# Performance work log

Measured on AMD Instinct MI355X. Metric: run time of the kernel, lower is better.

## Reference

```python
import jax, jax.numpy as jnp
import numpy as np

B, N, IN_DIM, HID, OUT, E = 2, 50000, 64, 256, 128, 500000

def setup_inputs() -> dict:
    key = jax.random.key(0)
    ks = jax.random.split(key, 8)
    s = lambda fan_in: 1.0 / np.sqrt(fan_in)
    x = jax.random.normal(ks[0], (B, N, IN_DIM), dtype=jnp.float32)
    edges = jax.random.randint(ks[1], (E, 2), 0, N, dtype=jnp.int64)
    return {
        "x": x,
        "edges": edges,
        "ew1": jax.random.normal(ks[2], (2 * IN_DIM, HID), dtype=jnp.float32) * s(2 * IN_DIM),
        "eb1": jnp.zeros((HID,), jnp.float32),
        "ew2": jax.random.normal(ks[3], (HID, OUT), dtype=jnp.float32) * s(HID),
        "eb2": jnp.zeros((OUT,), jnp.float32),
        "nw1": jax.random.normal(ks[4], (IN_DIM, HID), dtype=jnp.float32) * s(IN_DIM),
        "nb1": jnp.zeros((HID,), jnp.float32),
        "nw2": jax.random.normal(ks[5], (HID, OUT), dtype=jnp.float32) * s(HID),
        "nb2": jnp.zeros((OUT,), jnp.float32),
        "dw": jax.random.normal(ks[6], (OUT, IN_DIM), dtype=jnp.float32) * s(OUT),
        "db": jnp.zeros((IN_DIM,), jnp.float32),
    }

def _mlp(z, w1, b1, w2, b2):
    return jax.nn.relu(z @ w1 + b1) @ w2 + b2

def reference(x, edges, ew1, eb1, ew2, eb2, nw1, nb1, nw2, nb2, dw, db):
    u, v = edges[:, 0], edges[:, 1]
    # node embedding: [B, N, OUT]
    h = _mlp(x, nw1, nb1, nw2, nb2)
    # per-edge MLP on concatenated endpoint features: [B, E, OUT]
    edge_input = jnp.concatenate([x[:, u], x[:, v]], axis=-1)  # [B, E, 2*IN]
    edge_emb = _mlp(edge_input, ew1, eb1, ew2, eb2)
    # scatter-add edge message to both endpoints
    messages = jnp.zeros_like(h).at[:, u].add(edge_emb).at[:, v].add(edge_emb)
    h = h + messages
    recon = h @ dw + db  # [B, N, IN]
    return recon
```

## Files before the change

### kernel.cpp

```cpp
#include <hip/hip_runtime.h>
#include <hip/hip_bf16.h>

#define BB   2
#define NN   50000
#define BN   100000
#define NE   500000
#define NSB  196

using u16 = unsigned short;
using u32 = unsigned int;
typedef __attribute__((ext_vector_type(8))) short short8;
typedef __attribute__((ext_vector_type(8))) _Float16 half8;
typedef __attribute__((ext_vector_type(4))) float f32x4;

__device__ __forceinline__ u16 f2bf(float f) {
    union { float f; u32 u; } w; w.f = f;
    return (u16)((w.u + 0x7fffu + ((w.u >> 16) & 1u)) >> 16);
}
__device__ __forceinline__ u16 f2h(float f) {
    _Float16 h = (_Float16)f; u16 u; __builtin_memcpy(&u, &h, 2); return u;
}

#if defined(__has_builtin)
#if __has_builtin(__builtin_amdgcn_cvt_pk_bf16_f32)
#define HAVE_CVTPK 1
#endif
#if __has_builtin(__builtin_amdgcn_cvt_pkrtz)
#define HAVE_PKRTZ 1
#endif
#endif

__device__ __forceinline__ u32 pack_bf(float lo, float hi) {
#ifdef HAVE_CVTPK
    auto r = __builtin_amdgcn_cvt_pk_bf16_f32(lo, hi);
    u32 out; __builtin_memcpy(&out, &r, sizeof(out));
    return out;
#else
    return ((u32)f2bf(hi) << 16) | (u32)f2bf(lo);
#endif
}

__device__ __forceinline__ u32 pack_h2(float lo, float hi) {
#ifdef HAVE_PKRTZ
    auto r = __builtin_amdgcn_cvt_pkrtz(lo, hi);
    u32 out; __builtin_memcpy(&out, &r, sizeof(out));
    return out;
#else
    return ((u32)f2h(hi) << 16) | (u32)f2h(lo);
#endif
}

__device__ __forceinline__ u32 pk_add_h2(u32 a, u32 b) {
    u32 d; asm("v_pk_add_f16 %0, %1, %2" : "=v"(d) : "v"(a), "v"(b)); return d;
}
__device__ __forceinline__ u32 pk_relu_h2(u32 a) {
    u32 d, z = 0u;
    asm("v_pk_max_f16 %0, %1, %2" : "=v"(d) : "v"(a), "v"(z)); return d;
}
__device__ __forceinline__ half8 as_h8(short8 s) {
    half8 h; __builtin_memcpy(&h, &s, 16); return h;
}

__global__ __launch_bounds__(256) void csr_zero2(int* __restrict__ a, int* __restrict__ b) {
    int i = blockIdx.x * 256 + threadIdx.x;
    if (i < NN) { a[i] = 0; b[i] = 0; }
}

__global__ __launch_bounds__(256) void csr_hist2(const int* __restrict__ edges,
                                                 int* __restrict__ curU,
                                                 int* __restrict__ curV) {
    int e = blockIdx.x * 256 + threadIdx.x;
    if (e < NE) {
        atomicAdd(&curU[edges[2*e]], 1);
        atomicAdd(&curV[edges[2*e+1]], 1);
    }
}

__global__ __launch_bounds__(256) void scan_pass1(const int* __restrict__ cursor,
                                                  int* __restrict__ bsum) {
    __shared__ int s[256];
    const int t = threadIdx.x;
    int i = blockIdx.x * 256 + t;
    s[t] = (i < NN) ? cursor[i] : 0;
    __syncthreads();
    for (int d = 128; d > 0; d >>= 1) {
        if (t < d) s[t] += s[t + d];
        __syncthreads();
    }
    if (t == 0) bsum[blockIdx.x] = s[0];
}

__global__ __launch_bounds__(256) void scan_pass2(const int* __restrict__ bsum,
                                                  int* __restrict__ boff) {
    __shared__ int s[256];
    const int t = threadIdx.x;
    s[t] = (t < NSB) ? bsum[t] : 0;
    __syncthreads();
    for (int d = 1; d < 256; d <<= 1) {
        int v = (t >= d) ? s[t - d] : 0;
        __syncthreads();
        s[t] += v;
        __syncthreads();
    }
    if (t <= NSB) boff[t] = (t == 0) ? 0 : s[t - 1];
}

__global__ __launch_bounds__(256) void scan_pass3(int* __restrict__ cursor,
                                                  const int* __restrict__ boff,
                                                  int* __restrict__ off) {
    __shared__ int s[256];
    const int t = threadIdx.x;
    int i = blockIdx.x * 256 + t;
    int v = (i < NN) ? cursor[i] : 0;
    s[t] = v;
    __syncthreads();
    for (int d = 1; d < 256; d <<= 1) {
        int p = (t >= d) ? s[t - d] : 0;
        __syncthreads();
        s[t] += p;
        __syncthreads();
    }
    int excl = boff[blockIdx.x] + s[t] - v;
    if (i < NN) { off[i] = excl; cursor[i] = excl; }
    if (i == NN - 1) off[NN] = excl + v;
}

__global__ __launch_bounds__(256) void csr_fillU(const int* __restrict__ edges,
                                                 int* __restrict__ curU,
                                                 int* __restrict__ ueidx,
                                                 int* __restrict__ upos) {
    int e = blockIdx.x * 256 + threadIdx.x;
    if (e < NE) {
        int s = atomicAdd(&curU[edges[2*e]], 1);
        ueidx[s] = e;
        upos[e] = s;
    }
}

__global__ __launch_bounds__(256) void csr_fillV(const int* __restrict__ edges,
                                                 int* __restrict__ curV,
                                                 const int* __restrict__ upos,
                                                 int* __restrict__ vmap) {
    int e = blockIdx.x * 256 + threadIdx.x;
    if (e < NE) {
        int s = atomicAdd(&curV[edges[2*e+1]], 1);
        vmap[s] = upos[e];
    }
}

__global__ __launch_bounds__(256) void weight_prep(
    const float* __restrict__ ew1, const float* __restrict__ nw1,
    const float* __restrict__ ew2, const float* __restrict__ nw2,
    const float* __restrict__ dw,  const float* __restrict__ db,
    const float* __restrict__ eb2, const float* __restrict__ nb2,
    u16* __restrict__ frag, float* __restrict__ bias2)
{
    int blk = blockIdx.x, t = threadIdx.x;
    if (blk < 192) {
        int idx = blk * 256 + t;
        const float* src; int KB, local;
        if (idx < 32768) { local = idx;         src = ew1; KB = 4; }
        else             { local = idx - 32768; src = nw1; KB = 2; }
        int j = local & 7, l = (local >> 3) & 63, rest = local >> 9;
        int kblk = rest % KB, ntile = rest / KB;
        int n = ntile * 16 + (l & 15);
        int k = kblk * 32 + ((l >> 4) << 3) + j;
        frag[idx] = f2bf(src[k * 256 + n]);
    } else if (blk < 320) {
        int idx = (blk - 192) * 256 + t;
        bool is_e = (idx < 16384);
        const float* src = is_e ? ew2 : nw2;
        int local = idx & 16383;
        int j = local & 7, l = (local >> 3) & 63, rest = local >> 9;
        int kblk = rest & 7, ntile = rest >> 3;
        int n = ntile * 16 + (l & 15);
        int k = kblk * 32 + ((l >> 4) << 3) + j;
        float s = 0.f;
        for (int jj = 0; jj < 128; ++jj) s = fmaf(src[k * 128 + jj], dw[jj * 64 + n], s);
        frag[49152 + idx] = is_e ? f2h(s) : f2bf(s);
    } else if (t < 128) {
        int d = t & 63;
        const float* bsrc = (t >= 64) ? nb2 : eb2;
        float s = 0.f;
        #pragma unroll 4
        for (int j = 0; j < 128; ++j) s = fmaf(bsrc[j], dw[j * 64 + d], s);
        if (t >= 64) bias2[64 + d] = s + db[d];
        else         bias2[d] = s;
    }
}

__global__ __launch_bounds__(256) void node_mlp_kernel(
    const float* __restrict__ x, const float* __restrict__ nb1,
    const float* __restrict__ bias2, const u16* __restrict__ frag,
    u16* __restrict__ xbf, float* __restrict__ out)
{
    __shared__ u16 xs[64 * 64];
    __shared__ u16 hid[64 * 256];
    const int t = threadIdx.x;
    const int wave = t >> 6, l = t & 63, lane15 = l & 15, quad = l >> 4;
    const int r0 = blockIdx.x * 64;
    const int valid = min(64, BN - r0);

    #pragma unroll
    for (int it = 0; it < 4; ++it) {
        int i = t + it * 256;
        int m = i >> 4, c4 = i & 15;
        int row = min(r0 + m, BN - 1);
        float4 g = ((const float4*)x)[(size_t)row * 16 + c4];
        uint2 q = make_uint2(pack_bf(g.x, g.y), pack_bf(g.z, g.w));
        int chunk = c4 >> 1;
        *(uint2*)(xs + m * 64 + ((chunk ^ (m & 7)) << 3) + (c4 & 1) * 4) = q;
        *(uint2*)(xbf + (size_t)row * 64 + c4 * 4) = q;
    }
    __syncthreads();

    {
        f32x4 acc[4][4];
        #pragma unroll
        for (int i = 0; i < 4; ++i)
            #pragma unroll
            for (int mt = 0; mt < 4; ++mt) acc[i][mt] = f32x4{0.f,0.f,0.f,0.f};
        const u16* w1 = frag + 32768;
        #pragma unroll
        for (int kblk = 0; kblk < 2; ++kblk) {
            short8 bf[4], af[4];
            int chunk = kblk * 4 + quad;
            #pragma unroll
            for (int mt = 0; mt < 4; ++mt) {
                int row = mt*16 + lane15;
                bf[mt] = *(const short8*)(xs + row * 64 + ((chunk ^ (row & 7)) << 3));
            }
            #pragma unroll
            for (int i = 0; i < 4; ++i)
                af[i] = *(const short8*)(w1 + (((wave*4 + i)*2 + kblk)*64 + l) * 8);
            #pragma unroll
            for (int i = 0; i < 4; ++i)
                #pragma unroll
                for (int mt = 0; mt < 4; ++mt)
                    acc[i][mt] = __builtin_amdgcn_mfma_f32_16x16x32_bf16(af[i], bf[mt], acc[i][mt], 0, 0, 0);
        }
        #pragma unroll
        for (int i = 0; i < 4; ++i) {
            int n0 = (wave*4 + i)*16 + quad*4;
            int chunk = (wave*4 + i)*2 + (quad >> 1);
            float4 bv = *(const float4*)(nb1 + n0);
            #pragma unroll
            for (int mt = 0; mt < 4; ++mt) {
                int row = mt*16 + lane15;
                uint2 q = make_uint2(
                    pack_bf(fmaxf(acc[i][mt][0] + bv.x, 0.f), fmaxf(acc[i][mt][1] + bv.y, 0.f)),
                    pack_bf(fmaxf(acc[i][mt][2] + bv.z, 0.f), fmaxf(acc[i][mt][3] + bv.w, 0.f)));
                *(uint2*)(hid + row * 256 + ((chunk ^ (row & 15)) << 3) + (quad & 1) * 4) = q;
            }
        }
    }
    __syncthreads();

    {
        f32x4 acc[4];
        #pragma unroll
        for (int mt = 0; mt < 4; ++mt) acc[mt] = f32x4{0.f,0.f,0.f,0.f};
        const u16* w2 = frag + 65536;
        #pragma unroll
        for (int kblk = 0; kblk < 8; ++kblk) {
            short8 bf[4], af;
            int chunk = kblk * 4 + quad;
            #pragma unroll
            for (int mt = 0; mt < 4; ++mt) {
                int row = mt*16 + lane15;
                bf[mt] = *(const short8*)(hid + row * 256 + ((chunk ^ (row & 15)) << 3));
            }
            af = *(const short8*)(w2 + ((wave*8 + kblk)*64 + l) * 8);
            #pragma unroll
            for (int mt = 0; mt < 4; ++mt)
                acc[mt] = __builtin_amdgcn_mfma_f32_16x16x32_bf16(af, bf[mt], acc[mt], 0, 0, 0);
        }
        int n0 = wave*16 + quad*4;
        float4 bv = *(const float4*)(bias2 + 64 + n0);
        #pragma unroll
        for (int mt = 0; mt < 4; ++mt) {
            int m = mt*16 + lane15;
            if (m < valid) {
                float4 o;
                o.x = acc[mt][0] + bv.x; o.y = acc[mt][1] + bv.y;
                o.z = acc[mt][2] + bv.z; o.w = acc[mt][3] + bv.w;
                *(float4*)(out + (size_t)(r0 + m) * 64 + n0) = o;
            }
        }
    }
}

__global__ __launch_bounds__(256) void edge_pre_kernel(
    const u16* __restrict__ xbf, const float* __restrict__ eb1,
    const u16* __restrict__ frag, u16* __restrict__ At, u16* __restrict__ Ab,
    int b)
{
    __shared__ u16 xs[64 * 64];
    __shared__ u16 stg[64 * 256];
    const int t = threadIdx.x;
    const int wave = t >> 6, l = t & 63, lane15 = l & 15, quad = l >> 4;
    const int r0 = blockIdx.x * 64;
    const int valid = min(64, NN - r0);

    #pragma unroll
    for (int it = 0; it < 2; ++it) {
        int i = t + it * 256;
        int m = i >> 3, c = i & 7;
        int row = min(r0 + m, NN - 1);
        uint4 q = ((const uint4*)xbf)[((size_t)(b * NN + row)) * 8 + c];
        *(uint4*)(xs + m * 64 + ((c ^ (m & 7)) << 3)) = q;
    }
    __syncthreads();

    const u16* w1 = frag;
    for (int T = 0; T < 2; ++T) {
        f32x4 acc[4][4];
        #pragma unroll
        for (int i = 0; i < 4; ++i)
            #pragma unroll
            for (int mt = 0; mt < 4; ++mt) acc[i][mt] = f32x4{0.f,0.f,0.f,0.f};
        #pragma unroll
        for (int kblk = 0; kblk < 2; ++kblk) {
            short8 bf[4], af[4];
            int chunk = kblk * 4 + quad;
            #pragma unroll
            for (int mt = 0; mt < 4; ++mt) {
                int row = mt*16 + lane15;
                bf[mt] = *(const short8*)(xs + row * 64 + ((chunk ^ (row & 7)) << 3));
            }
            #pragma unroll
            for (int i = 0; i < 4; ++i)
                af[i] = *(const short8*)(w1 + (((wave*4 + i)*4 + T*2 + kblk)*64 + l) * 8);
            #pragma unroll
            for (int i = 0; i < 4; ++i)
                #pragma unroll
                for (int mt = 0; mt < 4; ++mt)
                    acc[i][mt] = __builtin_amdgcn_mfma_f32_16x16x32_bf16(af[i], bf[mt], acc[i][mt], 0, 0, 0);
        }
        #pragma unroll
        for (int i = 0; i < 4; ++i) {
            int ntile = wave*4 + i;
            int n0 = ntile*16 + quad*4;
            float4 bv;
            if (T == 0) bv = *(const float4*)(eb1 + n0);
            else        bv = make_float4(0.f, 0.f, 0.f, 0.f);
            int c16 = ntile*2 + (quad >> 1);
            #pragma unroll
            for (int mt = 0; mt < 4; ++mt) {
                int row = mt*16 + lane15;
                uint2 q = make_uint2(
                    pack_h2(acc[i][mt][0] + bv.x, acc[i][mt][1] + bv.y),
                    pack_h2(acc[i][mt][2] + bv.z, acc[i][mt][3] + bv.w));
                *(uint2*)(stg + row * 256 + ((c16 ^ (row & 7)) << 3) + (quad & 1) * 4) = q;
            }
        }
        __syncthreads();
        u16* dst = (T == 0) ? At : Ab;
        #pragma unroll
        for (int it = 0; it < 8; ++it) {
            int i = t + it * 256;
            int m = i >> 5, c = i & 31;
            if (m < valid)
                ((uint4*)dst)[((size_t)(r0 + m)) * 32 + c] =
                    *(const uint4*)(stg + m * 256 + ((c ^ (m & 7)) << 3));
        }
        __syncthreads();
    }
}

__global__ __launch_bounds__(256) void edge_emb2_kernel(
    const u16* __restrict__ At, const u16* __restrict__ Ab,
    const int* __restrict__ edges, const int* __restrict__ ueidx,
    const float* __restrict__ bias2,
    const u16* __restrict__ frag, u16* __restrict__ perm)
{
    __shared__ u16 hid[64 * 128];
    __shared__ int us[64], vs[64];
    const int t = threadIdx.x;
    const int wave = t >> 6, l = t & 63, lane15 = l & 15, quad = l >> 4;
    const int e0 = blockIdx.x * 64;
    const int valid = min(64, NE - e0);

    if (t < 64) {
        int j = min(e0 + t, NE - 1);
        int e = ueidx[j];
        us[t] = edges[2 * e];
        vs[t] = edges[2 * e + 1];
    }
    __syncthreads();

    f32x4 acc[4];
    #pragma unroll
    for (int mt = 0; mt < 4; ++mt) acc[mt] = f32x4{0.f,0.f,0.f,0.f};
    const u16* w2 = frag + 49152;

    #pragma unroll
    for (int half = 0; half < 2; ++half) {
        #pragma unroll
        for (int it = 0; it < 4; ++it) {
            int i = t + it * 256;
            int m = i >> 4, c = i & 15;
            int cg = half * 16 + c;
            int u = us[m], v = vs[m];
            uint4 a = ((const uint4*)At)[(size_t)((u32)u) * 32 + cg];
            uint4 bq = ((const uint4*)Ab)[(size_t)((u32)v) * 32 + cg];
            uint4 r;
            r.x = pk_relu_h2(pk_add_h2(a.x, bq.x));
            r.y = pk_relu_h2(pk_add_h2(a.y, bq.y));
            r.z = pk_relu_h2(pk_add_h2(a.z, bq.z));
            r.w = pk_relu_h2(pk_add_h2(a.w, bq.w));
            *(uint4*)(hid + m * 128 + ((c ^ (m & 15)) << 3)) = r;
        }
        __syncthreads();

        #pragma unroll
        for (int kb = 0; kb < 4; ++kb) {
            short8 bf[4], af;
            int chunk = kb * 4 + quad;
            #pragma unroll
            for (int mt = 0; mt < 4; ++mt) {
                int row = mt*16 + lane15;
                bf[mt] = *(const short8*)(hid + row * 128 + ((chunk ^ (row & 15)) << 3));
            }
            af = *(const short8*)(w2 + ((wave*8 + half*4 + kb)*64 + l) * 8);
            #pragma unroll
            for (int mt = 0; mt < 4; ++mt)
                acc[mt] = __builtin_amdgcn_mfma_f32_16x16x32_f16(as_h8(af), as_h8(bf[mt]), acc[mt], 0, 0, 0);
        }
        __syncthreads();
    }

    {
        int n0 = wave*16 + quad*4;
        int chunk = wave*2 + (quad >> 1);
        float4 bv = *(const float4*)(bias2 + n0);
        #pragma unroll
        for (int mt = 0; mt < 4; ++mt) {
            int m = mt*16 + lane15;
            uint2 q = make_uint2(
                pack_bf(acc[mt][0] + bv.x, acc[mt][1] + bv.y),
                pack_bf(acc[mt][2] + bv.z, acc[mt][3] + bv.w));
            *(uint2*)(hid + m * 64 + ((chunk ^ (m & 7)) << 3) + (quad & 1) * 4) = q;
        }
    }
    __syncthreads();

    #pragma unroll
    for (int it = 0; it < 2; ++it) {
        int i = t + it * 256;
        int m = i >> 3, c8 = i & 7;
        if (m < valid)
            ((uint4*)perm)[((size_t)(e0 + m)) * 8 + c8] =
                *(const uint4*)(hid + m * 64 + ((c8 ^ (m & 7)) << 3));
    }
}

__global__ __launch_bounds__(256) void gather3_kernel(
    const u32* __restrict__ perm32, const int* __restrict__ uoff,
    const int* __restrict__ voff, const int* __restrict__ vmap,
    float* __restrict__ out, int b)
{
    const int t = threadIdx.x, wave = t >> 6, l = t & 63;
    const int n = blockIdx.x * 4 + wave;
    const int ub = uoff[n], ucnt = uoff[n + 1] - ub;
    const int vb = voff[n], vcnt = voff[n + 1] - vb;
    if ((ucnt | vcnt) == 0) return;
    const int slot = l >> 4, c8h = l & 15;
    float a0 = 0.f, a1 = 0.f, a2 = 0.f, a3 = 0.f;

    for (int j0 = 0; j0 < ucnt; j0 += 8) {
        int jA = j0 + slot, jB = j0 + 4 + slot;
        const u32* rpA = perm32 + (size_t)(ub + min(jA, ucnt - 1)) * 32 + 2 * c8h;
        const u32* rpB = perm32 + (size_t)(ub + min(jB, ucnt - 1)) * 32 + 2 * c8h;
        u32 wA0 = rpA[0], wA1 = rpA[1];
        u32 wB0 = rpB[0], wB1 = rpB[1];
        union { u32 u; float f; } x0, x1, x2, x3;
        if (jA < ucnt) {
            x0.u = wA0 << 16; x1.u = wA0 & 0xffff0000u;
            x2.u = wA1 << 16; x3.u = wA1 & 0xffff0000u;
            a0 += x0.f; a1 += x1.f; a2 += x2.f; a3 += x3.f;
        }
        if (jB < ucnt) {
            x0.u = wB0 << 16; x1.u = wB0 & 0xffff0000u;
            x2.u = wB1 << 16; x3.u = wB1 & 0xffff0000u;
            a0 += x0.f; a1 += x1.f; a2 += x2.f; a3 += x3.f;
        }
    }
    for (int j0 = 0; j0 < vcnt; j0 += 8) {
        int jA = j0 + slot, jB = j0 + 4 + slot;
        int pA = vmap[vb + min(jA, vcnt - 1)];
        int pB = vmap[vb + min(jB, vcnt - 1)];
        const u32* rpA = perm32 + (size_t)pA * 32 + 2 * c8h;
        const u32* rpB = perm32 + (size_t)pB * 32 + 2 * c8h;
        u32 wA0 = rpA[0], wA1 = rpA[1];
        u32 wB0 = rpB[0], wB1 = rpB[1];
        union { u32 u; float f; } x0, x1, x2, x3;
        if (jA < vcnt) {
            x0.u = wA0 << 16; x1.u = wA0 & 0xffff0000u;
            x2.u = wA1 << 16; x3.u = wA1 & 0xffff0000u;
            a0 += x0.f; a1 += x1.f; a2 += x2.f; a3 += x3.f;
        }
        if (jB < vcnt) {
            x0.u = wB0 << 16; x1.u = wB0 & 0xffff0000u;
            x2.u = wB1 << 16; x3.u = wB1 & 0xffff0000u;
            a0 += x0.f; a1 += x1.f; a2 += x2.f; a3 += x3.f;
        }
    }

    a0 += __shfl_xor(a0, 16); a1 += __shfl_xor(a1, 16);
    a2 += __shfl_xor(a2, 16); a3 += __shfl_xor(a3, 16);
    a0 += __shfl_xor(a0, 32); a1 += __shfl_xor(a1, 32);
    a2 += __shfl_xor(a2, 32); a3 += __shfl_xor(a3, 32);
    if (l < 16) {
        float4* p = (float4*)(out + (size_t)(b * NN + n) * 64 + 4 * l);
        float4 h = *p;
        h.x += a0; h.y += a1; h.z += a2; h.w += a3;
        *p = h;
    }
}

extern "C" void kernel_launch(void* const* d_in, const int* in_sizes, int n_in,
                              void* d_out, int out_size, void* d_ws, size_t ws_size,
                              hipStream_t stream) {
    const float* x     = (const float*)d_in[0];
    const int*   edges = (const int*)d_in[1];
    const float* ew1   = (const float*)d_in[2];
    const float* eb1   = (const float*)d_in[3];
    const float* ew2   = (const float*)d_in[4];
    const float* eb2   = (const float*)d_in[5];
    const float* nw1   = (const float*)d_in[6];
    const float* nb1   = (const float*)d_in[7];
    const float* nw2   = (const float*)d_in[8];
    const float* nb2   = (const float*)d_in[9];
    const float* dw    = (const float*)d_in[10];
    const float* db    = (const float*)d_in[11];
    float* out = (float*)d_out;

    char* w = (char*)d_ws;
    size_t o = 0;
    auto take = [&](size_t bytes) { char* p = w + o; o = (o + bytes + 511) & ~(size_t)511; return p; };
    u16*   frag   = (u16*)  take(81920 * 2);
    float* bias2  = (float*)take(128 * 4);
    int*   curU   = (int*)  take((size_t)NN * 4);
    int*   curV   = (int*)  take((size_t)NN * 4);
    int*   uoff   = (int*)  take((size_t)(NN + 1) * 4);
    int*   voff   = (int*)  take((size_t)(NN + 1) * 4);
    int*   bsum   = (int*)  take((size_t)(NSB + 1) * 4);
    int*   boff   = (int*)  take((size_t)(NSB + 1) * 4);
    int*   ueidx  = (int*)  take((size_t)NE * 4);
    int*   upos   = (int*)  take((size_t)NE * 4);
    int*   vmap   = (int*)  take((size_t)NE * 4);
    u16*   xbf    = (u16*)  take((size_t)BN * 64 * 2);
    u16*   At     = (u16*)  take((size_t)NN * 256 * 2);
    u16*   Ab     = (u16*)  take((size_t)NN * 256 * 2);
    u16*   perm   = (u16*)  take((size_t)NE * 64 * 2);

    csr_zero2<<<NSB, 256, 0, stream>>>(curU, curV);
    csr_hist2<<<(NE + 255) / 256, 256, 0, stream>>>(edges, curU, curV);
    scan_pass1<<<NSB, 256, 0, stream>>>(curU, bsum);
    scan_pass2<<<1, 256, 0, stream>>>(bsum, boff);
    scan_pass3<<<NSB, 256, 0, stream>>>(curU, boff, uoff);
    scan_pass1<<<NSB, 256, 0, stream>>>(curV, bsum);
    scan_pass2<<<1, 256, 0, stream>>>(bsum, boff);
    scan_pass3<<<NSB, 256, 0, stream>>>(curV, boff, voff);
    csr_fillU<<<(NE + 255) / 256, 256, 0, stream>>>(edges, curU, ueidx, upos);
    csr_fillV<<<(NE + 255) / 256, 256, 0, stream>>>(edges, curV, upos, vmap);

    weight_prep<<<321, 256, 0, stream>>>(ew1, nw1, ew2, nw2, dw, db, eb2, nb2, frag, bias2);

    node_mlp_kernel<<<(BN + 63) / 64, 256, 0, stream>>>(x, nb1, bias2, frag, xbf, out);

    for (int b = 0; b < BB; ++b) {
        edge_pre_kernel<<<(NN + 63) / 64, 256, 0, stream>>>(xbf, eb1, frag, At, Ab, b);
        edge_emb2_kernel<<<(NE + 63) / 64, 256, 0, stream>>>(At, Ab, edges, ueidx, bias2, frag, perm);
        gather3_kernel<<<NN / 4, 256, 0, stream>>>((const u32*)perm, uoff, voff, vmap, out, b);
    }
}
```

Baseline: 457.5 us.

## Fuse edge pre-projection into node MLP and gather both batches at once

The node MLP kernel now also computes the per-node edge first-layer projections (At/Ab) for both batches, reusing the x tile already in LDS, which removes the separate edge_pre kernel and the xbf round-trip. The edge kernel writes both batches interleaved into one wider perm buffer, so a single gather kernel accumulates both batches per node and reuses the CSR offsets and vmap reads. The CSR fill stores (u,v) pairs directly so the edge kernel avoids an indirect edges lookup, and the two scans are merged into 2D-grid launches. The fused path needs a larger workspace and falls back to the old path when the workspace is too small.

```diff
diff --git a/kernel.cpp b/kernel.cpp
--- a/kernel.cpp
+++ b/kernel.cpp
@@ -76,10 +76,12 @@
     }
 }
 
-__global__ __launch_bounds__(256) void scan_pass1(const int* __restrict__ cursor,
-                                                  int* __restrict__ bsum) {
+__global__ __launch_bounds__(256) void scan_pass1d(const int* __restrict__ curU,
+                                                   const int* __restrict__ curV,
+                                                   int* __restrict__ bsum2) {
     __shared__ int s[256];
     const int t = threadIdx.x;
+    const int* cursor = blockIdx.y ? curV : curU;
     int i = blockIdx.x * 256 + t;
     s[t] = (i < NN) ? cursor[i] : 0;
     __syncthreads();
@@ -87,14 +89,15 @@
         if (t < d) s[t] += s[t + d];
         __syncthreads();
     }
-    if (t == 0) bsum[blockIdx.x] = s[0];
-}
-
-__global__ __launch_bounds__(256) void scan_pass2(const int* __restrict__ bsum,
-                                                  int* __restrict__ boff) {
+    if (t == 0) bsum2[blockIdx.y * (NSB + 1) + blockIdx.x] = s[0];
+}
+
+__global__ __launch_bounds__(256) void scan_pass2d(const int* __restrict__ bsum2,
+                                                   int* __restrict__ boff2) {
     __shared__ int s[256];
     const int t = threadIdx.x;
-    s[t] = (t < NSB) ? bsum[t] : 0;
+    const int base = blockIdx.y * (NSB + 1);
+    s[t] = (t < NSB) ? bsum2[base + t] : 0;
     __syncthreads();
     for (int d = 1; d < 256; d <<= 1) {
         int v = (t >= d) ? s[t - d] : 0;
@@ -102,14 +105,19 @@
         s[t] += v;
         __syncthreads();
     }
-    if (t <= NSB) boff[t] = (t == 0) ? 0 : s[t - 1];
-}
-
-__global__ __launch_bounds__(256) void scan_pass3(int* __restrict__ cursor,
-                                                  const int* __restrict__ boff,
-                                                  int* __restrict__ off) {
+    if (t <= NSB) boff2[base + t] = (t == 0) ? 0 : s[t - 1];
+}
+
+__global__ __launch_bounds__(256) void scan_pass3d(int* __restrict__ curU,
+                                                   int* __restrict__ curV,
+                                                   const int* __restrict__ boff2,
+                                                   int* __restrict__ uoff,
+                                                   int* __restrict__ voff) {
     __shared__ int s[256];
     const int t = threadIdx.x;
+    int* cursor = blockIdx.y ? curV : curU;
+    int* off    = blockIdx.y ? voff : uoff;
+    const int base = blockIdx.y * (NSB + 1);
     int i = blockIdx.x * 256 + t;
     int v = (i < NN) ? cursor[i] : 0;
     s[t] = v;
@@ -120,19 +128,20 @@
         s[t] += p;
         __syncthreads();
     }
-    int excl = boff[blockIdx.x] + s[t] - v;
+    int excl = boff2[base + blockIdx.x] + s[t] - v;
     if (i < NN) { off[i] = excl; cursor[i] = excl; }
     if (i == NN - 1) off[NN] = excl + v;
 }
 
 __global__ __launch_bounds__(256) void csr_fillU(const int* __restrict__ edges,
                                                  int* __restrict__ curU,
-                                                 int* __restrict__ ueidx,
+                                                 int2* __restrict__ uv,
                                                  int* __restrict__ upos) {
     int e = blockIdx.x * 256 + threadIdx.x;
     if (e < NE) {
-        int s = atomicAdd(&curU[edges[2*e]], 1);
-        ueidx[s] = e;
+        int u = edges[2*e], v = edges[2*e+1];
+        int s = atomicAdd(&curU[u], 1);
+        uv[s] = make_int2(u, v);
         upos[e] = s;
     }
 }
@@ -191,8 +200,10 @@
 
 __global__ __launch_bounds__(256) void node_mlp_kernel(
     const float* __restrict__ x, const float* __restrict__ nb1,
-    const float* __restrict__ bias2, const u16* __restrict__ frag,
-    u16* __restrict__ xbf, float* __restrict__ out)
+    const float* __restrict__ eb1, const float* __restrict__ bias2,
+    const u16* __restrict__ frag,
+    u16* __restrict__ xbf, u16* __restrict__ At, u16* __restrict__ Ab,
+    float* __restrict__ out, int emitAB)
 {
     __shared__ u16 xs[64 * 64];
     __shared__ u16 hid[64 * 256];
@@ -210,7 +221,7 @@
         uint2 q = make_uint2(pack_bf(g.x, g.y), pack_bf(g.z, g.w));
         int chunk = c4 >> 1;
         *(uint2*)(xs + m * 64 + ((chunk ^ (m & 7)) << 3) + (c4 & 1) * 4) = q;
-        *(uint2*)(xbf + (size_t)row * 64 + c4 * 4) = q;
+        if (!emitAB) *(uint2*)(xbf + (size_t)row * 64 + c4 * 4) = q;
     }
     __syncthreads();
 
@@ -287,6 +298,64 @@
                 *(float4*)(out + (size_t)(r0 + m) * 64 + n0) = o;
             }
         }
+    }
+
+    if (!emitAB) return;
+    __syncthreads();
+
+    const u16* w1 = frag;
+    for (int T = 0; T < 2; ++T) {
+        f32x4 acc[4][4];
+        #pragma unroll
+        for (int i = 0; i < 4; ++i)
+            #pragma unroll
+            for (int mt = 0; mt < 4; ++mt) acc[i][mt] = f32x4{0.f,0.f,0.f,0.f};
+        #pragma unroll
+        for (int kblk = 0; kblk < 2; ++kblk) {
+            short8 bf[4], af[4];
+            int chunk = kblk * 4 + quad;
+            #pragma unroll
+            for (int mt = 0; mt < 4; ++mt) {
+                int row = mt*16 + lane15;
+                bf[mt] = *(const short8*)(xs + row * 64 + ((chunk ^ (row & 7)) << 3));
+            }
+            #pragma unroll
+            for (int i = 0; i < 4; ++i)
+                af[i] = *(const short8*)(w1 + (((wave*4 + i)*4 + T*2 + kblk)*64 + l) * 8);
+            #pragma unroll
+            for (int i = 0; i < 4; ++i)
+                #pragma unroll
+                for (int mt = 0; mt < 4; ++mt)
+                    acc[i][mt] = __builtin_amdgcn_mfma_f32_16x16x32_bf16(af[i], bf[mt], acc[i][mt], 0, 0, 0);
+        }
+        #pragma unroll
+        for (int i = 0; i < 4; ++i) {
+            int ntile = wave*4 + i;
+            int n0 = ntile*16 + quad*4;
+            float4 bv;
+            if (T == 0) bv = *(const float4*)(eb1 + n0);
+            else        bv = make_float4(0.f, 0.f, 0.f, 0.f);
+            int c16 = ntile*2 + (quad >> 1);
+            #pragma unroll
+            for (int mt = 0; mt < 4; ++mt) {
+                int row = mt*16 + lane15;
+                uint2 q = make_uint2(
+                    pack_h2(acc[i][mt][0] + bv.x, acc[i][mt][1] + bv.y),
+                    pack_h2(acc[i][mt][2] + bv.z, acc[i][mt][3] + bv.w));
+                *(uint2*)(hid + row * 256 + ((c16 ^ (row & 7)) << 3) + (quad & 1) * 4) = q;
+            }
+        }
+        __syncthreads();
+        u16* dst = (T == 0) ? At : Ab;
+        #pragma unroll
+        for (int it = 0; it < 8; ++it) {
+            int i = t + it * 256;
+            int m = i >> 5, c = i & 31;
+            if (m < valid)
+                ((uint4*)dst)[((size_t)(r0 + m)) * 32 + c] =
+                    *(const uint4*)(hid + m * 256 + ((c ^ (m & 7)) << 3));
+        }
+        __syncthreads();
     }
 }
 
@@ -370,9 +439,9 @@
 
 __global__ __launch_bounds__(256) void edge_emb2_kernel(
     const u16* __restrict__ At, const u16* __restrict__ Ab,
-    const int* __restrict__ edges, const int* __restrict__ ueidx,
-    const float* __restrict__ bias2,
-    const u16* __restrict__ frag, u16* __restrict__ perm)
+    const int2* __restrict__ uv, const float* __restrict__ bias2,
+    const u16* __restrict__ frag, u16* __restrict__ perm,
+    int rowStride4, int dstOff4)
 {
     __shared__ u16 hid[64 * 128];
     __shared__ int us[64], vs[64];
@@ -382,10 +451,9 @@
     const int valid = min(64, NE - e0);
 
     if (t < 64) {
-        int j = min(e0 + t, NE - 1);
-        int e = ueidx[j];
-        us[t] = edges[2 * e];
-        vs[t] = edges[2 * e + 1];
+        int2 p = uv[min(e0 + t, NE - 1)];
+        us[t] = p.x;
+        vs[t] = p.y;
     }
     __syncthreads();
 
@@ -450,7 +518,7 @@
         int i = t + it * 256;
         int m = i >> 3, c8 = i & 7;
         if (m < valid)
-            ((uint4*)perm)[((size_t)(e0 + m)) * 8 + c8] =
+            ((uint4*)perm)[(size_t)(e0 + m) * rowStride4 + dstOff4 + c8] =
                 *(const uint4*)(hid + m * 64 + ((c8 ^ (m & 7)) << 3));
     }
 }
@@ -516,6 +584,64 @@
         float4 h = *p;
         h.x += a0; h.y += a1; h.z += a2; h.w += a3;
         *p = h;
+    }
+}
+
+#define ACCUM8(q) { union { u32 u; float f; } xx;                         \
+    xx.u = (q).x << 16;          a0 += xx.f;                              \
+    xx.u = (q).x & 0xffff0000u;  a1 += xx.f;                              \
+    xx.u = (q).y << 16;          a2 += xx.f;                              \
+    xx.u = (q).y & 0xffff0000u;  a3 += xx.f;                              \
+    xx.u = (q).z << 16;          a4 += xx.f;                              \
+    xx.u = (q).z & 0xffff0000u;  a5 += xx.f;                              \
+    xx.u = (q).w << 16;          a6 += xx.f;                              \
+    xx.u = (q).w & 0xffff0000u;  a7 += xx.f; }
+
+__global__ __launch_bounds__(256) void gather4_kernel(
+    const u32* __restrict__ perm32, const int* __restrict__ uoff,
+    const int* __restrict__ voff, const int* __restrict__ vmap,
+    float* __restrict__ out)
+{
+    const int t = threadIdx.x, wave = t >> 6, l = t & 63;
+    const int n = blockIdx.x * 4 + wave;
+    const int ub = uoff[n], ucnt = uoff[n + 1] - ub;
+    const int vb = voff[n], vcnt = voff[n + 1] - vb;
+    if ((ucnt | vcnt) == 0) return;
+    const int sg = l >> 4, c16 = l & 15;
+    float a0=0.f,a1=0.f,a2=0.f,a3=0.f,a4=0.f,a5=0.f,a6=0.f,a7=0.f;
+
+    for (int j0 = 0; j0 < ucnt; j0 += 8) {
+        int jA = j0 + sg, jB = j0 + 4 + sg;
+        uint4 qA = *(const uint4*)(perm32 + (size_t)(ub + min(jA, ucnt - 1)) * 64 + c16 * 4);
+        uint4 qB = *(const uint4*)(perm32 + (size_t)(ub + min(jB, ucnt - 1)) * 64 + c16 * 4);
+        if (jA < ucnt) ACCUM8(qA);
+        if (jB < ucnt) ACCUM8(qB);
+    }
+    for (int j0 = 0; j0 < vcnt; j0 += 8) {
+        int jA = j0 + sg, jB = j0 + 4 + sg;
+        int pA = vmap[vb + min(jA, vcnt - 1)];
+        int pB = vmap[vb + min(jB, vcnt - 1)];
+        uint4 qA = *(const uint4*)(perm32 + (size_t)pA * 64 + c16 * 4);
+        uint4 qB = *(const uint4*)(perm32 + (size_t)pB * 64 + c16 * 4);
+        if (jA < vcnt) ACCUM8(qA);
+        if (jB < vcnt) ACCUM8(qB);
+    }
+
+    a0 += __shfl_xor(a0, 16); a1 += __shfl_xor(a1, 16);
+    a2 += __shfl_xor(a2, 16); a3 += __shfl_xor(a3, 16);
+    a4 += __shfl_xor(a4, 16); a5 += __shfl_xor(a5, 16);
+    a6 += __shfl_xor(a6, 16); a7 += __shfl_xor(a7, 16);
+    a0 += __shfl_xor(a0, 32); a1 += __shfl_xor(a1, 32);
+    a2 += __shfl_xor(a2, 32); a3 += __shfl_xor(a3, 32);
+    a4 += __shfl_xor(a4, 32); a5 += __shfl_xor(a5, 32);
+    a6 += __shfl_xor(a6, 32); a7 += __shfl_xor(a7, 32);
+
+    if (l < 16) {
+        float* p = out + ((size_t)((l >> 3) * NN + n)) * 64 + (l & 7) * 8;
+        float4 h0 = *(float4*)p, h1 = *(float4*)(p + 4);
+        h0.x += a0; h0.y += a1; h0.z += a2; h0.w += a3;
+        h1.x += a4; h1.y += a5; h1.z += a6; h1.w += a7;
+        *(float4*)p = h0; *(float4*)(p + 4) = h1;
     }
 }
 
@@ -545,34 +671,53 @@
     int*   curV   = (int*)  take((size_t)NN * 4);
     int*   uoff   = (int*)  take((size_t)(NN + 1) * 4);
     int*   voff   = (int*)  take((size_t)(NN + 1) * 4);
-    int*   bsum   = (int*)  take((size_t)(NSB + 1) * 4);
-    int*   boff   = (int*)  take((size_t)(NSB + 1) * 4);
-    int*   ueidx  = (int*)  take((size_t)NE * 4);
+    int*   bsum2  = (int*)  take((size_t)2 * (NSB + 1) * 4);
+    int*   boff2  = (int*)  take((size_t)2 * (NSB + 1) * 4);
     int*   upos   = (int*)  take((size_t)NE * 4);
     int*   vmap   = (int*)  take((size_t)NE * 4);
-    u16*   xbf    = (u16*)  take((size_t)BN * 64 * 2);
-    u16*   At     = (u16*)  take((size_t)NN * 256 * 2);
-    u16*   Ab     = (u16*)  take((size_t)NN * 256 * 2);
-    u16*   perm   = (u16*)  take((size_t)NE * 64 * 2);
+    int2*  uv     = (int2*) take((size_t)NE * 8);
+    size_t oCommon = o;
+
+    u16* At   = (u16*)take((size_t)BN * 256 * 2);
+    u16* Ab   = (u16*)take((size_t)BN * 256 * 2);
+    u16* perm = (u16*)take((size_t)NE * 128 * 2);
+    bool fused = (o <= ws_size);
+
+    u16 *xbf = nullptr;
+    if (!fused) {
+        o = oCommon;
+        xbf  = (u16*)take((size_t)BN * 64 * 2);
+        At   = (u16*)take((size_t)NN * 256 * 2);
+        Ab   = (u16*)take((size_t)NN * 256 * 2);
+        perm = (u16*)take((size_t)NE * 64 * 2);
+    }
 
     csr_zero2<<<NSB, 256, 0, stream>>>(curU, curV);
     csr_hist2<<<(NE + 255) / 256, 256, 0, stream>>>(edges, curU, curV);
-    scan_pass1<<<NSB, 256, 0, stream>>>(curU, bsum);
-    scan_pass2<<<1, 256, 0, stream>>>(bsum, boff);
-    scan_pass3<<<NSB, 256, 0, stream>>>(curU, boff, uoff);
-    scan_pass1<<<NSB, 256, 0, stream>>>(curV, bsum);
-    scan_pass2<<<1, 256, 0, stream>>>(bsum, boff);
-    scan_pass3<<<NSB, 256, 0, stream>>>(curV, boff, voff);
-    csr_fillU<<<(NE + 255) / 256, 256, 0, stream>>>(edges, curU, ueidx, upos);
+    scan_pass1d<<<dim3(NSB, 2), 256, 0, stream>>>(curU, curV, bsum2);
+    scan_pass2d<<<dim3(1, 2), 256, 0, stream>>>(bsum2, boff2);
+    scan_pass3d<<<dim3(NSB, 2), 256, 0, stream>>>(curU, curV, boff2, uoff, voff);
+    csr_fillU<<<(NE + 255) / 256, 256, 0, stream>>>(edges, curU, uv, upos);
     csr_fillV<<<(NE + 255) / 256, 256, 0, stream>>>(edges, curV, upos, vmap);
 
     weight_prep<<<321, 256, 0, stream>>>(ew1, nw1, ew2, nw2, dw, db, eb2, nb2, frag, bias2);
 
-    node_mlp_kernel<<<(BN + 63) / 64, 256, 0, stream>>>(x, nb1, bias2, frag, xbf, out);
-
-    for (int b = 0; b < BB; ++b) {
-        edge_pre_kernel<<<(NN + 63) / 64, 256, 0, stream>>>(xbf, eb1, frag, At, Ab, b);
-        edge_emb2_kernel<<<(NE + 63) / 64, 256, 0, stream>>>(At, Ab, edges, ueidx, bias2, frag, perm);
-        gather3_kernel<<<NN / 4, 256, 0, stream>>>((const u32*)perm, uoff, voff, vmap, out, b);
-    }
-}
+    node_mlp_kernel<<<(BN + 63) / 64, 256, 0, stream>>>(
+        x, nb1, eb1, bias2, frag, xbf, At, Ab, out, fused ? 1 : 0);
+
+    if (fused) {
+        for (int b = 0; b < BB; ++b) {
+            edge_emb2_kernel<<<(NE + 63) / 64, 256, 0, stream>>>(
+                At + (size_t)b * NN * 256, Ab + (size_t)b * NN * 256,
+                uv, bias2, frag, perm, 16, b * 8);
+        }
+        gather4_kernel<<<NN / 4, 256, 0, stream>>>((const u32*)perm, uoff, voff, vmap, out);
+    } else {
+        for (int b = 0; b < BB; ++b) {
+            edge_pre_kernel<<<(NN + 63) / 64, 256, 0, stream>>>(xbf, eb1, frag, At, Ab, b);
+            edge_emb2_kernel<<<(NE + 63) / 64, 256, 0, stream>>>(
+                At, Ab, uv, bias2, frag, perm, 8, 0);
+            gather3_kernel<<<NN / 4, 256, 0, stream>>>((const u32*)perm, uoff, voff, vmap, out, b);
+        }
+    }
+}
```

New measurement: 419.1 us. 1.09x faster.
